# Kernel optimization log

Measured on AMD Instinct MI355X. Metric: run time of the kernel, lower is better.

## Reference

```python
import jax, jax.numpy as jnp
import numpy as np

# Config (matches init_kwargs)
B, L, D = 2, 2048, 1024
QH, KVH, HD, FFN = 8, 2, 128, 4096
EPS = 1.1920929e-07  # torch RMSNorm default eps = finfo(float32).eps


def _rope_ts():
    d2 = HD // 2
    freq_exp = (2.0 / HD) * jnp.arange(d2, dtype=jnp.float32)
    return 10000.0 ** freq_exp  # [d2]


def _rope(x):
    # x: [B, L, H, HD], rotated in fp32 (matches x.float() in source)
    d2 = HD // 2
    pos = jnp.arange(L, dtype=jnp.float32)
    rad = pos[:, None] / _rope_ts()[None, :]          # [L, d2]
    s = jnp.sin(rad)[None, :, None, :]                # [1, L, 1, d2]
    c = jnp.cos(rad)[None, :, None, :]
    xf = x.astype(jnp.float32)
    x1, x2 = xf[..., :d2], xf[..., d2:]
    return jnp.concatenate([x1 * c - x2 * s, x2 * c + x1 * s], axis=-1).astype(x.dtype)


def _rmsnorm(x, w):
    xf = x.astype(jnp.float32)
    r = jax.lax.rsqrt(jnp.mean(xf * xf, axis=-1, keepdims=True) + EPS)
    return (xf * r).astype(x.dtype) * w


def setup_inputs() -> dict:
    key = jax.random.key(0)
    ks = jax.random.split(key, 9)
    s = 0.02
    return {
        "x": jax.random.normal(ks[0], (B, L, D), dtype=jnp.float32),
        "ln1_w": jnp.ones((D,), dtype=jnp.float32),
        "wq": jax.random.normal(ks[1], (D, QH * HD), dtype=jnp.float32) * s,
        "wk": jax.random.normal(ks[2], (D, KVH * HD), dtype=jnp.float32) * s,
        "wv": jax.random.normal(ks[3], (D, KVH * HD), dtype=jnp.float32) * s,
        "wo": jax.random.normal(ks[4], (QH * HD, D), dtype=jnp.float32) * s,
        "ln2_w": jnp.ones((D,), dtype=jnp.float32),
        "wg": jax.random.normal(ks[5], (D, FFN), dtype=jnp.float32) * s,
        "wu": jax.random.normal(ks[6], (D, FFN), dtype=jnp.float32) * s,
        "wd": jax.random.normal(ks[7], (FFN, D), dtype=jnp.float32) * s,
    }


def reference(x, ln1_w, wq, wk, wv, wo, ln2_w, wg, wu, wd):
    residual = x
    h = _rmsnorm(x, ln1_w)

    q = _rope((h @ wq).reshape(B, L, QH, HD))          # [B,L,QH,HD]
    k = _rope((h @ wk).reshape(B, L, KVH, HD))         # [B,L,KVH,HD]
    v = (h @ wv).reshape(B, L, KVH, HD)

    rep = QH // KVH  # kv_map = floor(arange(QH)*KVH/QH) == repeat each kv head `rep` times
    qh = jnp.transpose(q, (0, 2, 1, 3)).astype(jnp.float32)                       # [B,QH,L,HD]
    kh = jnp.transpose(jnp.repeat(k, rep, axis=2), (0, 2, 1, 3)).astype(jnp.float32)
    vh = jnp.transpose(jnp.repeat(v, rep, axis=2), (0, 2, 1, 3)).astype(jnp.float32)

    scores = jnp.einsum("bhqd,bhkd->bhqk", qh, kh) / jnp.sqrt(jnp.float32(HD))    # [B,QH,L,L]
    causal = jnp.triu(jnp.ones((L, L), dtype=bool), 1)
    scores = jnp.where(causal, -jnp.inf, scores)
    attn = jax.nn.softmax(scores, axis=-1)
    ctx = jnp.einsum("bhqk,bhkd->bhqd", attn, vh)                                 # [B,QH,L,HD]
    ctx = jnp.transpose(ctx, (0, 2, 1, 3)).reshape(B, L, QH * HD).astype(x.dtype)

    x = ctx @ wo + residual
    residual = x
    h = _rmsnorm(x, ln2_w)
    return (jax.nn.silu(h @ wg) * (h @ wu)) @ wd + residual
```

## Files before the change

kernel.cpp:

```cpp
#include <hip/hip_runtime.h>
#include <hip/hip_bf16.h>
#include <math.h>

#define B_ 2
#define L_ 2048
#define D_ 1024
#define QH_ 8
#define KVH_ 2
#define HD_ 128
#define FFN_ 4096
#define T_ (B_ * L_)
#define EPS_ 1.1920929e-07f

typedef __bf16 bf16x8 __attribute__((ext_vector_type(8)));
typedef float floatx4 __attribute__((ext_vector_type(4)));
typedef unsigned short ushortx8 __attribute__((ext_vector_type(8)));
typedef unsigned short ushortx4 __attribute__((ext_vector_type(4)));

__device__ __forceinline__ unsigned short f2bf(float f) {
  union { float f; unsigned int u; } v;
  v.f = f;
  unsigned int r = v.u + 0x7FFFu + ((v.u >> 16) & 1u);
  return (unsigned short)(r >> 16);
}
__device__ __forceinline__ float bf2f(unsigned short u) {
  union { unsigned int u; float f; } v;
  v.u = ((unsigned int)u) << 16;
  return v.f;
}
__device__ __forceinline__ void gload_lds16(const void* g, void* l) {
  __builtin_amdgcn_global_load_lds((const __attribute__((address_space(1))) void*)g,
                                   (__attribute__((address_space(3))) void*)l, 16, 0, 0);
}

__device__ __forceinline__ void strip_tc(const float* __restrict__ in,
                                         unsigned short* __restrict__ out,
                                         int K, int N, int n0, int k0) {
  __shared__ float tile[4][32][33];
  int t = threadIdx.x;
  int tx = t & 31, ty = t >> 5;
#pragma unroll
  for (int s = 0; s < 4; s++)
#pragma unroll
    for (int r0 = 0; r0 < 4; r0++) {
      int r = ty + r0 * 8;
      tile[s][r][tx] = in[(size_t)(k0 + s * 32 + r) * N + n0 + tx];
    }
  __syncthreads();
  int nr = t >> 3, kq = t & 7;
#pragma unroll
  for (int s = 0; s < 4; s++) {
    ushortx4 o4;
#pragma unroll
    for (int j = 0; j < 4; j++) o4[j] = f2bf(tile[s][kq * 4 + j][nr]);
    *(ushortx4*)(out + (size_t)(n0 + nr) * K + k0 + s * 32 + kq * 4) = o4;
  }
}

__device__ __forceinline__ void rmsnorm_row(const float* __restrict__ x,
                                            const float* __restrict__ w,
                                            unsigned short* __restrict__ o, int row) {
  __shared__ float red[4];
  int t = threadIdx.x;
  const float* xr = x + (size_t)row * D_;
  float4 xv = *(const float4*)(xr + t * 4);
  float ss = xv.x * xv.x + xv.y * xv.y + xv.z * xv.z + xv.w * xv.w;
#pragma unroll
  for (int off = 32; off >= 1; off >>= 1) ss += __shfl_xor(ss, off);
  if ((t & 63) == 0) red[t >> 6] = ss;
  __syncthreads();
  float total = red[0] + red[1] + red[2] + red[3];
  float r = rsqrtf(total * (1.0f / (float)D_) + EPS_);
  float4 wv = *(const float4*)(w + t * 4);
  unsigned short* op = o + (size_t)row * D_ + t * 4;
  op[0] = f2bf(xv.x * r * wv.x);
  op[1] = f2bf(xv.y * r * wv.y);
  op[2] = f2bf(xv.z * r * wv.z);
  op[3] = f2bf(xv.w * r * wv.w);
}

__global__ __launch_bounds__(256) void prep_all(
    const float* __restrict__ wq, const float* __restrict__ wk,
    const float* __restrict__ wv, const float* __restrict__ wo,
    const float* __restrict__ wg, const float* __restrict__ wu,
    const float* __restrict__ wd, unsigned short* __restrict__ wT,
    const float* __restrict__ x, const float* __restrict__ ln1w,
    unsigned short* __restrict__ h_bf) {
  int bid = blockIdx.x;
  if (bid < 3712) {
    const float* in;
    unsigned short* out;
    int K, N, nt, base;
    if (bid < 256)       { in = wq; out = wT;            K = 1024; N = 1024; nt = 32;  base = 0; }
    else if (bid < 320)  { in = wk; out = wT + 1048576;  K = 1024; N = 256;  nt = 8;   base = 256; }
    else if (bid < 384)  { in = wv; out = wT + 1310720;  K = 1024; N = 256;  nt = 8;   base = 320; }
    else if (bid < 640)  { in = wo; out = wT + 1572864;  K = 1024; N = 1024; nt = 32;  base = 384; }
    else if (bid < 1664) { in = wg; out = wT + 2621440;  K = 1024; N = 4096; nt = 128; base = 640; }
    else if (bid < 2688) { in = wu; out = wT + 6815744;  K = 1024; N = 4096; nt = 128; base = 1664; }
    else                 { in = wd; out = wT + 11010048; K = 4096; N = 1024; nt = 32;  base = 2688; }
    int idx = bid - base;
    strip_tc(in, out, K, N, (idx % nt) * 32, (idx / nt) * 128);
  } else {
    rmsnorm_row(x, ln1w, h_bf, bid - 3712);
  }
}

__global__ __launch_bounds__(256) void rmsnorm_bf16_kernel(const float* __restrict__ x,
                                                           const float* __restrict__ w,
                                                           unsigned short* __restrict__ o) {
  rmsnorm_row(x, w, o, blockIdx.x);
}

template <int EPI, int KH>
__global__ __launch_bounds__(256, 3) void gemm_bf16(const unsigned short* __restrict__ A,
                                                    const unsigned short* __restrict__ BT,
                                                    const float* __restrict__ R,
                                                    float* __restrict__ C,
                                                    int M, int N, int K) {
  __shared__ unsigned short As[KH][64 * 32];
  __shared__ unsigned short Bs[KH][128 * 32];
  int t = threadIdx.x;
  int lane = t & 63, wave = t >> 6;
  int m0 = blockIdx.y * 64, n0 = blockIdx.x * 128;

  int row_a = t >> 2;
  int kc = ((t & 3) ^ ((t >> 3) & 3)) * 8;
  const unsigned short* ga0 = A + (size_t)(m0 + row_a) * K + kc;
  const unsigned short* gb0 = BT + (size_t)(n0 + row_a) * K + kc;
  const unsigned short* gb1 = BT + (size_t)(n0 + 64 + row_a) * K + kc;

  int wm = (wave & 1) * 32, wn = (wave >> 1) * 64;
  int fr = lane & 15, quad = lane >> 4;
  int sw = (quad ^ ((fr >> 1) & 3)) * 8;

  floatx4 acc[2][4];
#pragma unroll
  for (int i = 0; i < 2; i++)
#pragma unroll
    for (int j = 0; j < 4; j++) acc[i][j] = (floatx4){0.f, 0.f, 0.f, 0.f};

  for (int k0 = 0; k0 < K; k0 += 32 * KH) {
#pragma unroll
    for (int h = 0; h < KH; h++) {
      int ko = k0 + h * 32;
      gload_lds16(ga0 + ko, As[h] + wave * 512);
      gload_lds16(gb0 + ko, Bs[h] + wave * 512);
      gload_lds16(gb1 + ko, Bs[h] + 2048 + wave * 512);
    }
    __syncthreads();
#pragma unroll
    for (int h = 0; h < KH; h++) {
      const unsigned short* arp = As[h] + (size_t)(wm + fr) * 32 + sw;
      const unsigned short* brp = Bs[h] + (size_t)(wn + fr) * 32 + sw;
      bf16x8 af[2], bfr[4];
#pragma unroll
      for (int i = 0; i < 2; i++)
        af[i] = __builtin_bit_cast(bf16x8, *(const ushortx8*)(arp + i * 16 * 32));
#pragma unroll
      for (int j = 0; j < 4; j++)
        bfr[j] = __builtin_bit_cast(bf16x8, *(const ushortx8*)(brp + j * 16 * 32));
#pragma unroll
      for (int i = 0; i < 2; i++)
#pragma unroll
        for (int j = 0; j < 4; j++)
          acc[i][j] = __builtin_amdgcn_mfma_f32_16x16x32_bf16(af[i], bfr[j], acc[i][j], 0, 0, 0);
    }
    __syncthreads();
  }

  int orow = m0 + wm + quad * 4;
  int ocol = n0 + wn + fr;
#pragma unroll
  for (int i = 0; i < 2; i++) {
#pragma unroll
    for (int r = 0; r < 4; r++) {
      int row = orow + i * 16 + r;
#pragma unroll
      for (int j = 0; j < 4; j++) {
        size_t idx = (size_t)row * N + ocol + j * 16;
        float v = acc[i][j][r];
        if (EPI == 1) C[idx] = v + R[idx];
        else C[idx] = v + C[idx];
      }
    }
  }
}

__global__ __launch_bounds__(256) void gemm_qkv(const unsigned short* __restrict__ A,
                                                const unsigned short* __restrict__ BT,
                                                unsigned short* __restrict__ qb,
                                                unsigned short* __restrict__ Kb,
                                                unsigned short* __restrict__ Vt) {
  constexpr int K = 1024;
  __shared__ unsigned short smem[24576];
  int t = threadIdx.x;
  int lane = t & 63, wave = t >> 6;
  int bx = blockIdx.x;
  int m0 = blockIdx.y * 64, n0 = bx * 128;

  int row_a = t >> 2;
  int kc = ((t & 3) ^ ((t >> 3) & 3)) * 8;
  const unsigned short* ga0 = A + (size_t)(m0 + row_a) * K + kc;
  const unsigned short* gb0 = BT + (size_t)(n0 + row_a) * K + kc;
  const unsigned short* gb1 = BT + (size_t)(n0 + 64 + row_a) * K + kc;

  int wm = (wave & 1) * 32, wn = (wave >> 1) * 64;
  int fr = lane & 15, quad = lane >> 4;
  int sw = (quad ^ ((fr >> 1) & 3)) * 8;

  floatx4 acc[2][4];
#pragma unroll
  for (int i = 0; i < 2; i++)
#pragma unroll
    for (int j = 0; j < 4; j++) acc[i][j] = (floatx4){0.f, 0.f, 0.f, 0.f};

  for (int k0 = 0; k0 < K; k0 += 128) {
#pragma unroll
    for (int h = 0; h < 4; h++) {
      int ko = k0 + h * 32;
      gload_lds16(ga0 + ko, smem + h * 2048 + wave * 512);
      gload_lds16(gb0 + ko, smem + 8192 + h * 4096 + wave * 512);
      gload_lds16(gb1 + ko, smem + 8192 + h * 4096 + 2048 + wave * 512);
    }
    __syncthreads();
#pragma unroll
    for (int h = 0; h < 4; h++) {
      const unsigned short* arp = smem + h * 2048 + (size_t)(wm + fr) * 32 + sw;
      const unsigned short* brp = smem + 8192 + h * 4096 + (size_t)(wn + fr) * 32 + sw;
      bf16x8 af[2], bfr[4];
#pragma unroll
      for (int i = 0; i < 2; i++)
        af[i] = __builtin_bit_cast(bf16x8, *(const ushortx8*)(arp + i * 16 * 32));
#pragma unroll
      for (int j = 0; j < 4; j++)
        bfr[j] = __builtin_bit_cast(bf16x8, *(const ushortx8*)(brp + j * 16 * 32));
#pragma unroll
      for (int i = 0; i < 2; i++)
#pragma unroll
        for (int j = 0; j < 4; j++)
          acc[i][j] = __builtin_amdgcn_mfma_f32_16x16x32_bf16(af[i], bfr[j], acc[i][j], 0, 0, 0);
    }
    __syncthreads();
  }

  unsigned short* scr = smem;
#pragma unroll
  for (int i = 0; i < 2; i++)
#pragma unroll
    for (int r = 0; r < 4; r++)
#pragma unroll
      for (int j = 0; j < 4; j++)
        scr[(size_t)(wm + quad * 4 + i * 16 + r) * 136 + wn + fr + j * 16] =
            f2bf(acc[i][j][r]);
  __syncthreads();

  if (bx < 10) {
    int row = t >> 2, dq = (t & 3) * 16;
    int tok = m0 + row, pos = tok & (L_ - 1), b = tok >> 11;
    float scale_ = (bx < 8) ? 0.08838834764831843f : 1.0f;
    unsigned short lo[16], hi[16];
#pragma unroll
    for (int m = 0; m < 16; m++) {
      int d2 = dq + m;
      float x1 = bf2f(scr[(size_t)row * 136 + d2]);
      float x2 = bf2f(scr[(size_t)row * 136 + d2 + 64]);
      float inv_ts = expf(-0.14391156831f * (float)d2);
      float rad = (float)pos * inv_ts;
      float s = sinf(rad), c = cosf(rad);
      lo[m] = f2bf((x1 * c - x2 * s) * scale_);
      hi[m] = f2bf((x2 * c + x1 * s) * scale_);
    }
    if (bx < 8) {
      unsigned short* dst = qb + (size_t)tok * 1024 + bx * 128;
      *(ushortx8*)(dst + dq) = *(const ushortx8*)(lo);
      *(ushortx8*)(dst + dq + 8) = *(const ushortx8*)(lo + 8);
      *(ushortx8*)(dst + 64 + dq) = *(const ushortx8*)(hi);
      *(ushortx8*)(dst + 64 + dq + 8) = *(const ushortx8*)(hi + 8);
    } else {
      int kvh = bx - 8, bk = b * KVH_ + kvh, swk = pos & 15;
      unsigned short* dst = Kb + ((size_t)bk * L_ + pos) * HD_;
      int c0 = dq >> 3;
      *(ushortx8*)(dst + ((c0) ^ swk) * 8) = *(const ushortx8*)(lo);
      *(ushortx8*)(dst + ((c0 + 1) ^ swk) * 8) = *(const ushortx8*)(lo + 8);
      *(ushortx8*)(dst + ((c0 + 8) ^ swk) * 8) = *(const ushortx8*)(hi);
      *(ushortx8*)(dst + ((c0 + 9) ^ swk) * 8) = *(const ushortx8*)(hi + 8);
    }
  } else {
    int kvh = bx - 10;
    int b = m0 >> 11, key0 = m0 & (L_ - 1), bk = b * KVH_ + kvh;
    int hd = t >> 1, half = t & 1;
#pragma unroll
    for (int c = 0; c < 4; c++) {
      int cp = half * 4 + c, kcc = cp ^ (hd & 7);
      ushortx8 ob;
#pragma unroll
      for (int j = 0; j < 8; j++) ob[j] = scr[(size_t)(kcc * 8 + j) * 136 + hd];
      *(ushortx8*)(Vt + ((size_t)bk * HD_ + hd) * L_ + key0 + cp * 8) = ob;
    }
  }
}

__global__ __launch_bounds__(256, 2) void gemm_gateup3(
    const unsigned short* __restrict__ A,
    const unsigned short* __restrict__ BgT,
    const unsigned short* __restrict__ BuT,
    unsigned short* __restrict__ Cb) {
  constexpr int K = 1024;
  constexpr int NT = 32;
  __shared__ unsigned short As[3][128 * 32];
  __shared__ unsigned short Bs[3][256 * 32];

  int t = threadIdx.x;
  int lane = t & 63, wave = t >> 6;
  int m0 = blockIdx.y * 128;
  int n0l = blockIdx.x * 128;

  int row_a = t >> 2;
  int kc = ((t & 3) ^ ((t >> 3) & 3)) * 8;
  const unsigned short* ga0 = A + (size_t)(m0 + row_a) * K + kc;
  const unsigned short* ga1 = ga0 + (size_t)64 * K;
  const unsigned short* gb[4];
#pragma unroll
  for (int q = 0; q < 4; q++) {
    int rb = q * 64 + row_a;
    const unsigned short* src = ((rb & 31) < 16) ? BgT : BuT;
    gb[q] = src + (size_t)(n0l + (rb >> 5) * 16 + (rb & 15)) * K + kc;
  }

  int fr = lane & 15, quad = lane >> 4;
  int sw = (quad ^ ((fr >> 1) & 3)) * 8;
  int wn = wave;

  floatx4 acc[8][4];
#pragma unroll
  for (int i = 0; i < 8; i++)
#pragma unroll
    for (int j = 0; j < 4; j++) acc[i][j] = (floatx4){0.f, 0.f, 0.f, 0.f};

#define GU_STAGE(kt_)                                       \
  {                                                         \
    int ko_ = (kt_) * 32;                                   \
    int bi_ = (kt_) % 3;                                    \
    gload_lds16(ga0 + ko_, As[bi_] + wave * 512);           \
    gload_lds16(ga1 + ko_, As[bi_] + 2048 + wave * 512);    \
    gload_lds16(gb[0] + ko_, Bs[bi_] + wave * 512);         \
    gload_lds16(gb[1] + ko_, Bs[bi_] + 2048 + wave * 512);  \
    gload_lds16(gb[2] + ko_, Bs[bi_] + 4096 + wave * 512);  \
    gload_lds16(gb[3] + ko_, Bs[bi_] + 6144 + wave * 512);  \
  }

#define GU_COMPUTE(kt_)                                                          \
  {                                                                              \
    const unsigned short* asr = As[(kt_) % 3];                                   \
    const unsigned short* bsr = Bs[(kt_) % 3] + wn * 64 * 32;                    \
    bf16x8 af[8], bfr[4];                                                        \
    _Pragma("unroll") for (int j = 0; j < 4; j++) bfr[j] = __builtin_bit_cast(   \
        bf16x8, *(const ushortx8*)(bsr + (size_t)(j * 16 + fr) * 32 + sw));      \
    _Pragma("unroll") for (int i = 0; i < 8; i++) af[i] = __builtin_bit_cast(    \
        bf16x8, *(const ushortx8*)(asr + (size_t)(i * 16 + fr) * 32 + sw));      \
    __builtin_amdgcn_s_setprio(1);                                               \
    _Pragma("unroll") for (int i = 0; i < 8; i++)                                \
        _Pragma("unroll") for (int j = 0; j < 4; j++) acc[i][j] =                \
            __builtin_amdgcn_mfma_f32_16x16x32_bf16(af[i], bfr[j], acc[i][j],    \
                                                    0, 0, 0);                    \
    __builtin_amdgcn_s_setprio(0);                                               \
  }

  GU_STAGE(0);
  GU_STAGE(1);

  for (int kt = 0; kt < NT - 1; kt++) {
    asm volatile("s_waitcnt vmcnt(6)" ::: "memory");
    __builtin_amdgcn_s_barrier();
    asm volatile("" ::: "memory");
    if (kt < NT - 2) GU_STAGE(kt + 2);
    GU_COMPUTE(kt);
  }
  asm volatile("s_waitcnt vmcnt(0)" ::: "memory");
  __builtin_amdgcn_s_barrier();
  asm volatile("" ::: "memory");
  GU_COMPUTE(NT - 1);

#undef GU_STAGE
#undef GU_COMPUTE

#pragma unroll
  for (int i = 0; i < 8; i++) {
    int row = m0 + i * 16 + quad * 4;
#pragma unroll
    for (int r = 0; r < 4; r++) {
#pragma unroll
      for (int jj = 0; jj < 2; jj++) {
        float g = acc[i][2 * jj][r];
        float u = acc[i][2 * jj + 1][r];
        int colL = n0l + (wn * 2 + jj) * 16 + fr;
        Cb[(size_t)(row + r) * FFN_ + colL] = f2bf(g / (1.f + __expf(-g)) * u);
      }
    }
  }
}

__global__ __launch_bounds__(256) void attn_mfma(const unsigned short* __restrict__ qb,
                                                 const unsigned short* __restrict__ Kb,
                                                 const unsigned short* __restrict__ Vt,
                                                 unsigned short* __restrict__ ctx) {
  __shared__ unsigned short Ks[64 * 128];
  __shared__ unsigned short Vs[128 * 64];
  __shared__ unsigned short Ps[4][16 * 72];
  int id = blockIdx.x;
  int bh = id & 15;
  int p_ = id >> 4;
  int qt = (p_ < 16) ? p_ : 47 - p_;
  int b = bh >> 3, h = bh & 7;
  int bk = b * KVH_ + (h >> 2);
  int q0 = qt * 64;
  int t = threadIdx.x, lane = t & 63, w = t >> 6;
  int fr = lane & 15, quad = lane >> 4;

  int pos = q0 + w * 16 + fr;
  const unsigned short* qrow = qb + (size_t)(b * L_ + pos) * 1024 + h * HD_;
  bf16x8 qf[4];
#pragma unroll
  for (int kb = 0; kb < 4; kb++)
    qf[kb] = __builtin_bit_cast(bf16x8, *(const ushortx8*)(qrow + kb * 32 + quad * 8));

  floatx4 o_acc[8];
#pragma unroll
  for (int nt = 0; nt < 8; nt++) o_acc[nt] = (floatx4){0.f, 0.f, 0.f, 0.f};
  float l_r[4] = {0.f, 0.f, 0.f, 0.f};
  unsigned short* Psw = Ps[w];
  const unsigned short* kgb = Kb + (size_t)bk * L_ * HD_;
  const unsigned short* vgb = Vt + (size_t)bk * HD_ * L_;
  int rowg0 = q0 + w * 16 + quad * 4;

  for (int kt = 0; kt <= qt; kt++) {
    int kstart = kt * 64;
    bool diag = (kt == qt);
    __syncthreads();
    const unsigned short* ksrc = kgb + (size_t)kstart * HD_;
#pragma unroll
    for (int it = 0; it < 4; it++) {
      int sl = it * 4 + w;
      gload_lds16(ksrc + sl * 512 + lane * 8, Ks + sl * 512);
    }
#pragma unroll
    for (int it = 0; it < 4; it++) {
      int sl = it * 4 + w;
      gload_lds16(vgb + (size_t)(sl * 8 + (lane >> 3)) * L_ + kstart + (lane & 7) * 8,
                  Vs + sl * 512);
    }
    __syncthreads();

    floatx4 s_acc[4];
#pragma unroll
    for (int jt = 0; jt < 4; jt++) s_acc[jt] = (floatx4){0.f, 0.f, 0.f, 0.f};
#pragma unroll
    for (int kb = 0; kb < 4; kb++) {
#pragma unroll
      for (int jt = 0; jt < 4; jt++) {
        bf16x8 kf = __builtin_bit_cast(
            bf16x8, *(const ushortx8*)(Ks + (jt * 16 + fr) * 128 +
                                       (((kb * 4 + quad) ^ fr) * 8)));
        s_acc[jt] = __builtin_amdgcn_mfma_f32_16x16x32_bf16(qf[kb], kf, s_acc[jt], 0, 0, 0);
      }
    }

#pragma unroll
    for (int jt = 0; jt < 4; jt++) {
#pragma unroll
      for (int r = 0; r < 4; r++) {
        float pp;
        if (diag) {
          int keyg = kstart + jt * 16 + fr;
          pp = (keyg <= rowg0 + r) ? __expf(s_acc[jt][r]) : 0.f;
        } else {
          pp = __expf(s_acc[jt][r]);
        }
        l_r[r] += pp;
        Psw[(quad * 4 + r) * 72 + jt * 16 + fr] = f2bf(pp);
      }
    }
    bf16x8 pf0 = __builtin_bit_cast(bf16x8, *(const ushortx8*)(Psw + fr * 72 + quad * 8));
    bf16x8 pf1 =
        __builtin_bit_cast(bf16x8, *(const ushortx8*)(Psw + fr * 72 + 32 + quad * 8));
#pragma unroll
    for (int nt = 0; nt < 8; nt++) {
      bf16x8 vf0 = __builtin_bit_cast(
          bf16x8,
          *(const ushortx8*)(Vs + (nt * 16 + fr) * 64 + ((quad ^ (fr & 7)) * 8)));
      bf16x8 vf1 = __builtin_bit_cast(
          bf16x8,
          *(const ushortx8*)(Vs + (nt * 16 + fr) * 64 + (((4 + quad) ^ (fr & 7)) * 8)));
      o_acc[nt] = __builtin_amdgcn_mfma_f32_16x16x32_bf16(pf0, vf0, o_acc[nt], 0, 0, 0);
      o_acc[nt] = __builtin_amdgcn_mfma_f32_16x16x32_bf16(pf1, vf1, o_acc[nt], 0, 0, 0);
    }
  }

#pragma unroll
  for (int r = 0; r < 4; r++) {
    l_r[r] += __shfl_xor(l_r[r], 1);
    l_r[r] += __shfl_xor(l_r[r], 2);
    l_r[r] += __shfl_xor(l_r[r], 4);
    l_r[r] += __shfl_xor(l_r[r], 8);
  }

  unsigned short* ob =
      ctx + (size_t)(b * L_ + q0 + w * 16 + quad * 4) * 1024 + h * HD_ + fr;
#pragma unroll
  for (int r = 0; r < 4; r++) {
    float inv = 1.f / l_r[r];
    unsigned short* orow = ob + (size_t)r * 1024;
#pragma unroll
    for (int nt = 0; nt < 8; nt++) orow[nt * 16] = f2bf(o_acc[nt][r] * inv);
  }
}

extern "C" void kernel_launch(void* const* d_in, const int* in_sizes, int n_in,
                              void* d_out, int out_size, void* d_ws, size_t ws_size,
                              hipStream_t stream) {
  const float* x    = (const float*)d_in[0];
  const float* ln1w = (const float*)d_in[1];
  const float* wq   = (const float*)d_in[2];
  const float* wk   = (const float*)d_in[3];
  const float* wvp  = (const float*)d_in[4];
  const float* wo   = (const float*)d_in[5];
  const float* ln2w = (const float*)d_in[6];
  const float* wg   = (const float*)d_in[7];
  const float* wu   = (const float*)d_in[8];
  const float* wd   = (const float*)d_in[9];
  float* out = (float*)d_out;
  char* ws = (char*)d_ws;

  unsigned short* wT = (unsigned short*)ws;
  unsigned short* wqkvT = wT;
  unsigned short* woT = wT + 1572864;
  unsigned short* wgT = wT + 2621440;
  unsigned short* wuT = wT + 6815744;
  unsigned short* wdT = wT + 11010048;
  unsigned short* h_bf = (unsigned short*)(ws + 30408704);
  unsigned short* qb = (unsigned short*)(ws + 38797312);
  unsigned short* h2_bf = (unsigned short*)(ws + 51380224);
  unsigned short* Kb = (unsigned short*)(ws + 59768832);
  unsigned short* Vt = (unsigned short*)(ws + 61865984);
  unsigned short* gu = (unsigned short*)(ws + 59768832);
  unsigned short* ctx_bf = h_bf;

  dim3 blk(256);

  prep_all<<<3712 + T_, blk, 0, stream>>>(wq, wk, wvp, wo, wg, wu, wd, wT, x, ln1w, h_bf);
  gemm_qkv<<<dim3(12, 64), blk, 0, stream>>>(h_bf, wqkvT, qb, Kb, Vt);
  attn_mfma<<<512, blk, 0, stream>>>(qb, Kb, Vt, ctx_bf);
  gemm_bf16<1, 4><<<dim3(8, 64), blk, 0, stream>>>(ctx_bf, woT, x, out, T_, 1024, 1024);
  rmsnorm_bf16_kernel<<<T_, blk, 0, stream>>>(out, ln2w, h2_bf);
  gemm_gateup3<<<dim3(32, 32), blk, 0, stream>>>(h2_bf, wgT, wuT, gu);
  gemm_bf16<2, 4><<<dim3(8, 64), blk, 0, stream>>>(gu, wdT, nullptr, out, T_, 1024, FFN_);
}
```

Baseline: 368.5 us.

## Replace triple-buffered gate/up GEMM pipeline with synchronous two-stage K loop

The gate/up GEMM drops its three-stage async prefetch pipeline with vmcnt waits and priority hints. Each 64-wide K step now loads two 32-wide slabs into LDS, synchronizes, computes both, and synchronizes again. LDS use falls from three buffers to two, and launch bounds request three blocks per CU to raise occupancy. The cost is that global loads no longer overlap compute within a block, so the kernel relies on other resident blocks to hide memory latency.

Result: no change. 371.7 us (+0.9%).

```diff
diff --git a/kernel.cpp b/kernel.cpp
--- a/kernel.cpp
+++ b/kernel.cpp
@@ -300,15 +300,14 @@
   }
 }
 
-__global__ __launch_bounds__(256, 2) void gemm_gateup3(
+__global__ __launch_bounds__(256, 3) void gemm_gateup2(
     const unsigned short* __restrict__ A,
     const unsigned short* __restrict__ BgT,
     const unsigned short* __restrict__ BuT,
     unsigned short* __restrict__ Cb) {
   constexpr int K = 1024;
-  constexpr int NT = 32;
-  __shared__ unsigned short As[3][128 * 32];
-  __shared__ unsigned short Bs[3][256 * 32];
+  __shared__ unsigned short As[2][128 * 32];
+  __shared__ unsigned short Bs[2][256 * 32];
 
   int t = threadIdx.x;
   int lane = t & 63, wave = t >> 6;
@@ -337,52 +336,40 @@
 #pragma unroll
     for (int j = 0; j < 4; j++) acc[i][j] = (floatx4){0.f, 0.f, 0.f, 0.f};
 
-#define GU_STAGE(kt_)                                       \
-  {                                                         \
-    int ko_ = (kt_) * 32;                                   \
-    int bi_ = (kt_) % 3;                                    \
-    gload_lds16(ga0 + ko_, As[bi_] + wave * 512);           \
-    gload_lds16(ga1 + ko_, As[bi_] + 2048 + wave * 512);    \
-    gload_lds16(gb[0] + ko_, Bs[bi_] + wave * 512);         \
-    gload_lds16(gb[1] + ko_, Bs[bi_] + 2048 + wave * 512);  \
-    gload_lds16(gb[2] + ko_, Bs[bi_] + 4096 + wave * 512);  \
-    gload_lds16(gb[3] + ko_, Bs[bi_] + 6144 + wave * 512);  \
-  }
-
-#define GU_COMPUTE(kt_)                                                          \
-  {                                                                              \
-    const unsigned short* asr = As[(kt_) % 3];                                   \
-    const unsigned short* bsr = Bs[(kt_) % 3] + wn * 64 * 32;                    \
-    bf16x8 af[8], bfr[4];                                                        \
-    _Pragma("unroll") for (int j = 0; j < 4; j++) bfr[j] = __builtin_bit_cast(   \
-        bf16x8, *(const ushortx8*)(bsr + (size_t)(j * 16 + fr) * 32 + sw));      \
-    _Pragma("unroll") for (int i = 0; i < 8; i++) af[i] = __builtin_bit_cast(    \
-        bf16x8, *(const ushortx8*)(asr + (size_t)(i * 16 + fr) * 32 + sw));      \
-    __builtin_amdgcn_s_setprio(1);                                               \
-    _Pragma("unroll") for (int i = 0; i < 8; i++)                                \
-        _Pragma("unroll") for (int j = 0; j < 4; j++) acc[i][j] =                \
-            __builtin_amdgcn_mfma_f32_16x16x32_bf16(af[i], bfr[j], acc[i][j],    \
-                                                    0, 0, 0);                    \
-    __builtin_amdgcn_s_setprio(0);                                               \
-  }
-
-  GU_STAGE(0);
-  GU_STAGE(1);
-
-  for (int kt = 0; kt < NT - 1; kt++) {
-    asm volatile("s_waitcnt vmcnt(6)" ::: "memory");
-    __builtin_amdgcn_s_barrier();
-    asm volatile("" ::: "memory");
-    if (kt < NT - 2) GU_STAGE(kt + 2);
-    GU_COMPUTE(kt);
-  }
-  asm volatile("s_waitcnt vmcnt(0)" ::: "memory");
-  __builtin_amdgcn_s_barrier();
-  asm volatile("" ::: "memory");
-  GU_COMPUTE(NT - 1);
-
-#undef GU_STAGE
-#undef GU_COMPUTE
+  for (int k0 = 0; k0 < K; k0 += 64) {
+#pragma unroll
+    for (int h = 0; h < 2; h++) {
+      int ko = k0 + h * 32;
+      gload_lds16(ga0 + ko, As[h] + wave * 512);
+      gload_lds16(ga1 + ko, As[h] + 2048 + wave * 512);
+      gload_lds16(gb[0] + ko, Bs[h] + wave * 512);
+      gload_lds16(gb[1] + ko, Bs[h] + 2048 + wave * 512);
+      gload_lds16(gb[2] + ko, Bs[h] + 4096 + wave * 512);
+      gload_lds16(gb[3] + ko, Bs[h] + 6144 + wave * 512);
+    }
+    __syncthreads();
+#pragma unroll
+    for (int h = 0; h < 2; h++) {
+      const unsigned short* asr = As[h];
+      const unsigned short* bsr = Bs[h] + wn * 64 * 32;
+      bf16x8 af[8], bfr[4];
+#pragma unroll
+      for (int j = 0; j < 4; j++)
+        bfr[j] = __builtin_bit_cast(
+            bf16x8, *(const ushortx8*)(bsr + (size_t)(j * 16 + fr) * 32 + sw));
+#pragma unroll
+      for (int i = 0; i < 8; i++)
+        af[i] = __builtin_bit_cast(
+            bf16x8, *(const ushortx8*)(asr + (size_t)(i * 16 + fr) * 32 + sw));
+#pragma unroll
+      for (int i = 0; i < 8; i++)
+#pragma unroll
+        for (int j = 0; j < 4; j++)
+          acc[i][j] = __builtin_amdgcn_mfma_f32_16x16x32_bf16(af[i], bfr[j],
+                                                              acc[i][j], 0, 0, 0);
+    }
+    __syncthreads();
+  }
 
 #pragma unroll
   for (int i = 0; i < 8; i++) {
@@ -552,6 +539,6 @@
   attn_mfma<<<512, blk, 0, stream>>>(qb, Kb, Vt, ctx_bf);
   gemm_bf16<1, 4><<<dim3(8, 64), blk, 0, stream>>>(ctx_bf, woT, x, out, T_, 1024, 1024);
   rmsnorm_bf16_kernel<<<T_, blk, 0, stream>>>(out, ln2w, h2_bf);
-  gemm_gateup3<<<dim3(32, 32), blk, 0, stream>>>(h2_bf, wgT, wuT, gu);
+  gemm_gateup2<<<dim3(32, 32), blk, 0, stream>>>(h2_bf, wgT, wuT, gu);
   gemm_bf16<2, 4><<<dim3(8, 64), blk, 0, stream>>>(gu, wdT, nullptr, out, T_, 1024, FFN_);
 }
```
